# Performance work log

Measured on AMD Instinct MI355X. Metric: run time of the kernel, lower is better.

## Reference

```python
import jax, jax.numpy as jnp
import numpy as np

NG, CPN, K = 16, 24, 5          # ngroups, channels-per-group, kernel size
C = NG * CPN                     # 384 total channels
PAD = K // 2                     # PseudoEntropyPad(2, ...)


def build_mask():
    """PixelCNN-style group-causal mask for MaskConv2 (hidden/type-B: center
    position allows input group <= output group)."""
    m = np.zeros((C, C, K, K), np.float32)
    m[:, :, :PAD, :] = 1.0                      # rows above center: all allowed
    m[:, :, PAD, :PAD] = 1.0                    # center row, left of center
    g = np.arange(C) // CPN
    m[:, :, PAD, PAD] = (g[None, :] <= g[:, None]).astype(np.float32)
    return jnp.asarray(m)


def masked_conv(x, w, b, mask):
    # zero pad by 2 (PseudoEntropyPad) + VALID 5x5 conv == SAME conv
    y = jax.lax.conv_general_dilated(
        x, w * mask, window_strides=(1, 1), padding=[(PAD, PAD), (PAD, PAD)],
        dimension_numbers=("NCHW", "OIHW", "NCHW"))
    return y + b[None, :, None, None]


def prelu(x, a):
    return jnp.where(x >= 0, x, a[None, :, None, None] * x)


def setup_inputs() -> dict:
    key = jax.random.key(0)
    ks = jax.random.split(key, 5)
    x = jax.random.normal(ks[0], (2, C, 256, 512), dtype=jnp.float32)
    w1 = jax.random.normal(ks[1], (C, C, K, K), dtype=jnp.float32) * 0.02
    w2 = jax.random.normal(ks[2], (C, C, K, K), dtype=jnp.float32) * 0.02
    b1 = jnp.zeros((C,), jnp.float32)
    b2 = jnp.zeros((C,), jnp.float32)
    a1 = jnp.full((C,), 0.25, jnp.float32)   # PReLU init
    a2 = jnp.full((C,), 0.25, jnp.float32)
    return {"x": x, "w1": w1, "b1": b1, "a1": a1, "w2": w2, "b2": b2, "a2": a2}


def reference(x, w1, b1, a1, w2, b2, a2):
    mask = build_mask()
    y = prelu(masked_conv(x, w1, b1, mask), a1)   # EntropyConv 1 (pad+conv+PReLU+trim)
    y = prelu(masked_conv(y, w2, b2, mask), a2)   # EntropyConv 2
    return y + x                                   # residual
```

## Files before the change

### kernel.cpp

```cpp
#include <hip/hip_runtime.h>
#include <hip/hip_bf16.h>


#define C_CH 384
#define HH   256
#define WWD  512
#define NN   2
#define NKC  24
#define PR   260
#define PC   516
#define ICS16 (PR * PC * 16)
#define TCOLS 144
#define PLANE_SH (4 * TCOLS * 16)
#define TSH (2 * PLANE_SH)
#define TSTRIDE (NKC * C_CH * 16)
#define ICSTRIDE (2 * C_CH * 16)

typedef __attribute__((ext_vector_type(8)))  short short8;
typedef __attribute__((ext_vector_type(16))) float f32x16;

typedef const __attribute__((address_space(1))) void* gas_t;
typedef __attribute__((address_space(3))) void* las_t;

__device__ inline unsigned short f2bf(float f) {
    union { float f; unsigned int u; } v; v.f = f;
    unsigned int r = v.u + 0x7FFFu + ((v.u >> 16) & 1u);
    return (unsigned short)(r >> 16);
}

__global__ __launch_bounds__(256) void k_prepack(const float* __restrict__ w1, const float* __restrict__ w2,
                                                 unsigned short* __restrict__ wp1, unsigned short* __restrict__ wp2) {
    int idx = blockIdx.x * 256 + threadIdx.x;
    const int TOT = 13 * NKC * C_CH * 16;
    if (idx >= TOT) return;
    int iq = idx & 15;
    int o  = (idx >> 4) % C_CH;
    int kc = (idx / (16 * C_CH)) % NKC;
    int t  = idx / (16 * C_CH * NKC);
    int i  = kc * 16 + iq;
    int kh = t < 5 ? 0 : (t < 10 ? 1 : 2);
    int kw = t < 5 ? t : (t < 10 ? t - 5 : t - 10);
    bool keep = (t != 12) || ((i / 24) <= (o / 24));
    int src = ((o * C_CH + i) * 5 + kh) * 5 + kw;
    wp1[idx] = keep ? f2bf(w1[src]) : (unsigned short)0;
    wp2[idx] = keep ? f2bf(w2[src]) : (unsigned short)0;
}

__global__ __launch_bounds__(256) void k_zero_halo(unsigned short* __restrict__ a, unsigned short* __restrict__ b) {
    int plane = blockIdx.x;
    const short8 z = (short8){0,0,0,0,0,0,0,0};
    for (int bi = 0; bi < 2; ++bi) {
        unsigned short* p = (bi ? b : a) + (size_t)plane * ICS16;
        for (int i = threadIdx.x; i < 4128; i += 256) {
            int r4 = i / 1032;
            int rem = i - r4 * 1032;
            int row = r4 < 2 ? r4 : 254 + r4;
            *(short8*)&p[row * (PC * 16) + rem * 8] = z;
        }
        for (int i = threadIdx.x; i < 2048; i += 256) {
            int row = 2 + (i >> 3);
            int j = i & 7;
            int col = (j < 4) ? (j >> 1) : (512 + (j >> 1));
            int q = j & 1;
            *(short8*)&p[(row * PC + col) * 16 + q * 8] = z;
        }
    }
}

__global__ __launch_bounds__(256) void k_repack_x(const float* __restrict__ x, unsigned short* __restrict__ xc) {
    int bid = blockIdx.x;
    int w0 = (bid & 7) << 6;
    int h  = (bid >> 3) & 255;
    int n  = bid >> 11;
    int wi = threadIdx.x & 63;
    int cq = threadIdx.x >> 6;
    int w  = w0 + wi;
    int inb = n * C_CH * HH * WWD + h * WWD + w;
    for (int cc = 0; cc < 12; ++cc) {
        int c0 = cc * 32 + cq * 8;
        short8 outv;
        #pragma unroll
        for (int k = 0; k < 8; ++k) {
            float f = x[inb + (c0 + k) * (HH * WWD)];
            outv[k] = (short)f2bf(f);
        }
        int kc = cc * 2 + (cq >> 1);
        int oidx = (n * NKC + kc) * ICS16 + ((h + 2) * PC + (w + 2)) * 16 + (cq & 1) * 8;
        *(short8*)&xc[oidx] = outv;
    }
}

template<int SECOND>
__global__ __launch_bounds__(256, 2) void k_conv(const unsigned short* __restrict__ in,
                                                 const unsigned short* __restrict__ wp,
                                                 const float* __restrict__ bias,
                                                 const float* __restrict__ alpha,
                                                 const float* __restrict__ xres,
                                                 void* __restrict__ outp) {
    __shared__ __align__(16) unsigned short Xs[2][TSH];

    int bid0 = blockIdx.x;
    int xcd = bid0 & 7;
    int j0  = bid0 >> 3;
    int tile = xcd * 128 + j0 / 3;
    int ob   = j0 % 3;
    int n    = tile >> 9;
    int hp   = (tile >> 2) & 127;
    int wseg = tile & 3;
    int w0 = wseg << 7, o0 = ob << 7, h0 = hp << 1;

    int tid = threadIdx.x;
    int lane = tid & 63;
    int wv = tid >> 6;
    int wr = wv >> 1, wc = wv & 1;
    int lo5 = lane & 31, hi = lane >> 5;

    int goff[9];
    #pragma unroll
    for (int it = 0; it < 9; ++it) {
        int k = wv * 9 + it;
        int plane = k / 18;
        int s = (k % 18) * 64 + lane;
        int r = s / 288;
        int rem = s - r * 288;
        int col = rem >> 1, h16 = rem & 1;
        goff[it] = plane * ICS16 + ((h0 + r) * PC + (w0 + col)) * 16 + h16 * 8;
    }

    f32x16 acc[4][2];
    #pragma unroll
    for (int pt = 0; pt < 4; ++pt)
        #pragma unroll
        for (int ot = 0; ot < 2; ++ot)
            #pragma unroll
            for (int r = 0; r < 16; ++r) acc[pt][ot][r] = 0.f;

    const unsigned short* gbase_n = in + (size_t)n * NKC * ICS16;

    const int xlane = wr * (TCOLS * 16) + lo5 * 16 + hi * 8;
    const unsigned short* wpb = wp + (size_t)(o0 + wc * 64) * 16;
    const int wlane = lo5 * 16 + hi * 8;
    int woff0 = 0;
    int woff1 = C_CH * 16;

    const int KH[13] = {0,0,0,0,0,1,1,1,1,1,2,2,2};
    const int KW[13] = {0,1,2,3,4,0,1,2,3,4,0,1,2};

#define LOAD_XA(dst, u) do {                                              \
        const int t_ = (u) >> 1, hf_ = (u) & 1;                           \
        const int c0_ = hf_ * PLANE_SH + KH[t_] * (TCOLS * 16)            \
                      + KW[t_] * 16;                                      \
        _Pragma("unroll")                                                 \
        for (int pt_ = 0; pt_ < 4; ++pt_)                                 \
            (dst)[pt_] = *(const short8*)&xsp[xlane + c0_ + pt_ * 512];   \
    } while (0)

#define LOAD_WB(dst, woff) do {                                           \
        (dst)[0] = *(const short8*)&wpb[(woff) + wlane];                  \
        (dst)[1] = *(const short8*)&wpb[(woff) + wlane + 512];            \
    } while (0)

#define OCTET(xv, wv_) do {                                               \
        _Pragma("unroll")                                                 \
        for (int pt = 0; pt < 4; ++pt)                                    \
            _Pragma("unroll")                                             \
            for (int ot = 0; ot < 2; ++ot) {                              \
                if (SECOND)                                               \
                    acc[pt][ot] = __builtin_amdgcn_mfma_f32_32x32x16_bf16( \
                        (wv_)[ot], (xv)[pt], acc[pt][ot], 0, 0, 0);        \
                else                                                      \
                    acc[pt][ot] = __builtin_amdgcn_mfma_f32_32x32x16_bf16( \
                        (xv)[pt], (wv_)[ot], acc[pt][ot], 0, 0, 0);        \
            }                                                             \
    } while (0)

    short8 wb[2][2];
    LOAD_WB(wb[0], woff0);
    LOAD_WB(wb[1], woff1);

    #pragma unroll
    for (int it = 0; it < 9; ++it)
        __builtin_amdgcn_global_load_lds((gas_t)(gbase_n + goff[it]),
                                         (las_t)&Xs[0][(wv * 9 + it) * 512], 16, 0, 0);
    __syncthreads();

    for (int ic = 0; ic < 12; ++ic) {
        const unsigned short* xsp = &Xs[ic & 1][0];
        if (ic < 11) {
            const unsigned short* gb = gbase_n + (size_t)(ic + 1) * 2 * ICS16;
            #pragma unroll
            for (int it = 0; it < 9; ++it)
                __builtin_amdgcn_global_load_lds((gas_t)(gb + goff[it]),
                                                 (las_t)&Xs[(ic & 1) ^ 1][(wv * 9 + it) * 512], 16, 0, 0);
        }

        short8 xa[2][4];
        LOAD_XA(xa[0], 0);

        #pragma unroll
        for (int s2 = 0; s2 < 26; ++s2) {
            if (s2 + 1 < 26) LOAD_XA(xa[(s2 + 1) & 1], s2 + 1);
            __builtin_amdgcn_s_barrier();
            __builtin_amdgcn_s_setprio(1);
            OCTET(xa[s2 & 1], wb[s2 & 1]);
            __builtin_amdgcn_s_setprio(0);
            if (s2 + 2 < 26) {
                if ((s2 & 1) == 0) { woff0 += TSTRIDE; LOAD_WB(wb[0], woff0); }
                else               { woff1 += TSTRIDE; LOAD_WB(wb[1], woff1); }
            } else {
                if ((s2 & 1) == 0) { woff0 += ICSTRIDE - 12 * TSTRIDE; LOAD_WB(wb[0], woff0); }
                else               { woff1 += ICSTRIDE - 12 * TSTRIDE; LOAD_WB(wb[1], woff1); }
            }
        }
        __syncthreads();
    }
#undef LOAD_XA
#undef LOAD_WB
#undef OCTET

    int h = h0 + wr;
    if (!SECOND) {
        unsigned short* y = (unsigned short*)outp;
        #pragma unroll
        for (int ot = 0; ot < 2; ++ot) {
            int o = o0 + wc * 64 + ot * 32 + lo5;
            float bo = bias[o], ao = alpha[o];
            int kc = o >> 4;
            int o15 = o & 15;
            size_t base = (size_t)(n * NKC + kc) * ICS16 + ((h + 2) * PC + (w0 + 2)) * 16 + o15;
            #pragma unroll
            for (int pt = 0; pt < 4; ++pt) {
                #pragma unroll
                for (int reg = 0; reg < 16; ++reg) {
                    int p = pt * 32 + (reg & 3) + 8 * (reg >> 2) + 4 * hi;
                    float v = acc[pt][ot][reg] + bo;
                    v = v >= 0.f ? v : ao * v;
                    y[base + (size_t)p * 16] = f2bf(v);
                }
            }
        }
    } else {
        float* outf = (float*)outp;
        #pragma unroll
        for (int ot = 0; ot < 2; ++ot) {
            #pragma unroll
            for (int reg = 0; reg < 16; ++reg) {
                int o = o0 + wc * 64 + ot * 32 + (reg & 3) + 8 * (reg >> 2) + 4 * hi;
                float bo = bias[o], ao = alpha[o];
                #pragma unroll
                for (int pt = 0; pt < 4; ++pt) {
                    int w = w0 + pt * 32 + lo5;
                    float v = acc[pt][ot][reg] + bo;
                    v = v >= 0.f ? v : ao * v;
                    size_t idx = (size_t)((n * C_CH + o) * HH + h) * WWD + w;
                    outf[idx] = v + xres[idx];
                }
            }
        }
    }
}

extern "C" void kernel_launch(void* const* d_in, const int* in_sizes, int n_in,
                              void* d_out, int out_size, void* d_ws, size_t ws_size,
                              hipStream_t stream) {
    const float* x  = (const float*)d_in[0];
    const float* w1 = (const float*)d_in[1];
    const float* b1 = (const float*)d_in[2];
    const float* a1 = (const float*)d_in[3];
    const float* w2 = (const float*)d_in[4];
    const float* b2 = (const float*)d_in[5];
    const float* a2 = (const float*)d_in[6];

    const size_t PLANE_SHORTS = (size_t)NN * NKC * ICS16;
    unsigned short* xc  = (unsigned short*)d_out;
    unsigned short* yb  = (unsigned short*)d_ws;
    unsigned short* wp1 = yb + PLANE_SHORTS;
    unsigned short* wp2 = wp1 + 13 * NKC * C_CH * 16;

    k_prepack<<<(13 * NKC * C_CH * 16 + 255) / 256, 256, 0, stream>>>(w1, w2, wp1, wp2);
    k_zero_halo<<<NN * NKC, 256, 0, stream>>>(xc, yb);
    k_repack_x<<<NN * HH * (WWD / 64), 256, 0, stream>>>(x, xc);
    k_conv<0><<<3072, 256, 0, stream>>>(xc, wp1, b1, a1, nullptr, (void*)yb);
    k_conv<1><<<3072, 256, 0, stream>>>(yb, wp2, b2, a2, x, (void*)d_out);
}
```

Measured before the change: 1.801 ms.

## Shrink conv tile to one output row and stage per 16-channel chunk

The conv tile drops from two output rows by 128 columns to one row by 128 columns, and the grid doubles. Each wave now covers a 64-pixel by 64-channel quadrant, with half the accumulators. Input staging goes from two 16-channel planes per step to one plane over three rows, which shrinks LDS use and lets launch bounds target 4 blocks per SM. The aim is higher occupancy and better latency hiding, paid for with less reuse: each input row is now staged for only one output row, and weights are re-read twice as often per pixel.

```diff
diff --git a/kernel.cpp b/kernel.cpp
--- a/kernel.cpp
+++ b/kernel.cpp
@@ -10,11 +10,10 @@
 #define PR   260
 #define PC   516
 #define ICS16 (PR * PC * 16)
-#define TCOLS 144
-#define PLANE_SH (4 * TCOLS * 16)
-#define TSH (2 * PLANE_SH)
+#define TC3  160
+#define BUFSH (3 * TC3 * 16)
 #define TSTRIDE (NKC * C_CH * 16)
-#define ICSTRIDE (2 * C_CH * 16)
+#define CSTRIDE (C_CH * 16)
 
 typedef __attribute__((ext_vector_type(8)))  short short8;
 typedef __attribute__((ext_vector_type(16))) float f32x16;
@@ -91,45 +90,44 @@
 }
 
 template<int SECOND>
-__global__ __launch_bounds__(256, 2) void k_conv(const unsigned short* __restrict__ in,
+__global__ __launch_bounds__(256, 4) void k_conv(const unsigned short* __restrict__ in,
                                                  const unsigned short* __restrict__ wp,
                                                  const float* __restrict__ bias,
                                                  const float* __restrict__ alpha,
                                                  const float* __restrict__ xres,
                                                  void* __restrict__ outp) {
-    __shared__ __align__(16) unsigned short Xs[2][TSH];
+    __shared__ __align__(16) unsigned short Xs[2][BUFSH];
 
     int bid0 = blockIdx.x;
     int xcd = bid0 & 7;
     int j0  = bid0 >> 3;
-    int tile = xcd * 128 + j0 / 3;
+    int tile = xcd * 256 + j0 / 3;
     int ob   = j0 % 3;
-    int n    = tile >> 9;
-    int hp   = (tile >> 2) & 127;
     int wseg = tile & 3;
-    int w0 = wseg << 7, o0 = ob << 7, h0 = hp << 1;
+    int h0   = (tile >> 2) & 255;
+    int n    = tile >> 10;
+    int w0 = wseg << 7, o0 = ob << 7;
 
     int tid = threadIdx.x;
     int lane = tid & 63;
     int wv = tid >> 6;
-    int wr = wv >> 1, wc = wv & 1;
+    int pc = wv >> 1, oc = wv & 1;
     int lo5 = lane & 31, hi = lane >> 5;
 
-    int goff[9];
+    int goff[4];
     #pragma unroll
-    for (int it = 0; it < 9; ++it) {
-        int k = wv * 9 + it;
-        int plane = k / 18;
-        int s = (k % 18) * 64 + lane;
-        int r = s / 288;
-        int rem = s - r * 288;
-        int col = rem >> 1, h16 = rem & 1;
-        goff[it] = plane * ICS16 + ((h0 + r) * PC + (w0 + col)) * 16 + h16 * 8;
-    }
-
-    f32x16 acc[4][2];
+    for (int k = 0; k < 4; ++k) {
+        int i = wv + 4 * k;
+        int row = i / 5, cb = i % 5;
+        goff[k] = ((h0 + row) * PC + (w0 + cb * 32 + (lane >> 1))) * 16 + (lane & 1) * 8;
+    }
+
+    const int KH[13] = {0,0,0,0,0,1,1,1,1,1,2,2,2};
+    const int KW[13] = {0,1,2,3,4,0,1,2,3,4,0,1,2};
+
+    f32x16 acc[2][2];
     #pragma unroll
-    for (int pt = 0; pt < 4; ++pt)
+    for (int pt = 0; pt < 2; ++pt)
         #pragma unroll
         for (int ot = 0; ot < 2; ++ot)
             #pragma unroll
@@ -137,22 +135,27 @@
 
     const unsigned short* gbase_n = in + (size_t)n * NKC * ICS16;
 
-    const int xlane = wr * (TCOLS * 16) + lo5 * 16 + hi * 8;
-    const unsigned short* wpb = wp + (size_t)(o0 + wc * 64) * 16;
+    const int xlane = (pc * 64 + lo5) * 16 + hi * 8;
+    const unsigned short* wpb = wp + (size_t)(o0 + oc * 64) * 16;
     const int wlane = lo5 * 16 + hi * 8;
     int woff0 = 0;
-    int woff1 = C_CH * 16;
-
-    const int KH[13] = {0,0,0,0,0,1,1,1,1,1,2,2,2};
-    const int KW[13] = {0,1,2,3,4,0,1,2,3,4,0,1,2};
-
-#define LOAD_XA(dst, u) do {                                              \
-        const int t_ = (u) >> 1, hf_ = (u) & 1;                           \
-        const int c0_ = hf_ * PLANE_SH + KH[t_] * (TCOLS * 16)            \
-                      + KW[t_] * 16;                                      \
+    int woff1 = TSTRIDE;
+
+#define STAGE(kcn, b) do {                                                \
+        const unsigned short* gb_ = gbase_n + (size_t)(kcn) * ICS16;      \
         _Pragma("unroll")                                                 \
-        for (int pt_ = 0; pt_ < 4; ++pt_)                                 \
-            (dst)[pt_] = *(const short8*)&xsp[xlane + c0_ + pt_ * 512];   \
+        for (int k_ = 0; k_ < 4; ++k_) {                                  \
+            int i_ = wv + 4 * k_;                                         \
+            if (i_ < 15)                                                  \
+                __builtin_amdgcn_global_load_lds((gas_t)(gb_ + goff[k_]), \
+                    (las_t)&Xs[b][i_ * 512], 16, 0, 0);                   \
+        }                                                                 \
+    } while (0)
+
+#define LOAD_XA(dst, t_) do {                                             \
+        const int c0_ = (KH[t_] * TC3 + KW[t_]) * 16;                     \
+        (dst)[0] = *(const short8*)&xsp[xlane + c0_];                     \
+        (dst)[1] = *(const short8*)&xsp[xlane + c0_ + 512];               \
     } while (0)
 
 #define LOAD_WB(dst, woff) do {                                           \
@@ -160,79 +163,76 @@
         (dst)[1] = *(const short8*)&wpb[(woff) + wlane + 512];            \
     } while (0)
 
-#define OCTET(xv, wv_) do {                                               \
+#define QUAD(xv, wq) do {                                                 \
         _Pragma("unroll")                                                 \
-        for (int pt = 0; pt < 4; ++pt)                                    \
+        for (int pt = 0; pt < 2; ++pt)                                    \
             _Pragma("unroll")                                             \
             for (int ot = 0; ot < 2; ++ot) {                              \
                 if (SECOND)                                               \
                     acc[pt][ot] = __builtin_amdgcn_mfma_f32_32x32x16_bf16( \
-                        (wv_)[ot], (xv)[pt], acc[pt][ot], 0, 0, 0);        \
+                        (wq)[ot], (xv)[pt], acc[pt][ot], 0, 0, 0);         \
                 else                                                      \
                     acc[pt][ot] = __builtin_amdgcn_mfma_f32_32x32x16_bf16( \
-                        (xv)[pt], (wv_)[ot], acc[pt][ot], 0, 0, 0);        \
+                        (xv)[pt], (wq)[ot], acc[pt][ot], 0, 0, 0);         \
             }                                                             \
+    } while (0)
+
+#define HALF(bufi, wxor) do {                                             \
+        const unsigned short* xsp = &Xs[bufi][0];                         \
+        short8 xa[2][2];                                                  \
+        LOAD_XA(xa[0], 0);                                                \
+        _Pragma("unroll")                                                 \
+        for (int s2 = 0; s2 < 13; ++s2) {                                 \
+            if (s2 < 12) LOAD_XA(xa[(s2 + 1) & 1], s2 + 1);               \
+            __builtin_amdgcn_s_barrier();                                 \
+            __builtin_amdgcn_s_setprio(1);                                \
+            QUAD(xa[s2 & 1], wb[(s2 & 1) ^ (wxor)]);                      \
+            __builtin_amdgcn_s_setprio(0);                                \
+            if (((s2 & 1) ^ (wxor)) == 0) {                               \
+                woff0 += (s2 < 11) ? 2 * TSTRIDE : (CSTRIDE - 11 * TSTRIDE); \
+                LOAD_WB(wb[0], woff0);                                    \
+            } else {                                                      \
+                woff1 += (s2 < 11) ? 2 * TSTRIDE : (CSTRIDE - 11 * TSTRIDE); \
+                LOAD_WB(wb[1], woff1);                                    \
+            }                                                             \
+        }                                                                 \
     } while (0)
 
     short8 wb[2][2];
     LOAD_WB(wb[0], woff0);
     LOAD_WB(wb[1], woff1);
 
-    #pragma unroll
-    for (int it = 0; it < 9; ++it)
-        __builtin_amdgcn_global_load_lds((gas_t)(gbase_n + goff[it]),
-                                         (las_t)&Xs[0][(wv * 9 + it) * 512], 16, 0, 0);
+    STAGE(0, 0);
     __syncthreads();
 
-    for (int ic = 0; ic < 12; ++ic) {
-        const unsigned short* xsp = &Xs[ic & 1][0];
-        if (ic < 11) {
-            const unsigned short* gb = gbase_n + (size_t)(ic + 1) * 2 * ICS16;
-            #pragma unroll
-            for (int it = 0; it < 9; ++it)
-                __builtin_amdgcn_global_load_lds((gas_t)(gb + goff[it]),
-                                                 (las_t)&Xs[(ic & 1) ^ 1][(wv * 9 + it) * 512], 16, 0, 0);
-        }
-
-        short8 xa[2][4];
-        LOAD_XA(xa[0], 0);
-
-        #pragma unroll
-        for (int s2 = 0; s2 < 26; ++s2) {
-            if (s2 + 1 < 26) LOAD_XA(xa[(s2 + 1) & 1], s2 + 1);
-            __builtin_amdgcn_s_barrier();
-            __builtin_amdgcn_s_setprio(1);
-            OCTET(xa[s2 & 1], wb[s2 & 1]);
-            __builtin_amdgcn_s_setprio(0);
-            if (s2 + 2 < 26) {
-                if ((s2 & 1) == 0) { woff0 += TSTRIDE; LOAD_WB(wb[0], woff0); }
-                else               { woff1 += TSTRIDE; LOAD_WB(wb[1], woff1); }
-            } else {
-                if ((s2 & 1) == 0) { woff0 += ICSTRIDE - 12 * TSTRIDE; LOAD_WB(wb[0], woff0); }
-                else               { woff1 += ICSTRIDE - 12 * TSTRIDE; LOAD_WB(wb[1], woff1); }
-            }
-        }
+    for (int j = 0; j < 12; ++j) {
+        STAGE(2 * j + 1, 1);
+        HALF(0, 0);
         __syncthreads();
-    }
+        if (j < 11) STAGE(2 * j + 2, 0);
+        HALF(1, 1);
+        __syncthreads();
+    }
+#undef STAGE
 #undef LOAD_XA
 #undef LOAD_WB
-#undef OCTET
-
-    int h = h0 + wr;
+#undef QUAD
+#undef HALF
+
     if (!SECOND) {
         unsigned short* y = (unsigned short*)outp;
         #pragma unroll
         for (int ot = 0; ot < 2; ++ot) {
-            int o = o0 + wc * 64 + ot * 32 + lo5;
+            int o = o0 + oc * 64 + ot * 32 + lo5;
             float bo = bias[o], ao = alpha[o];
             int kc = o >> 4;
             int o15 = o & 15;
-            size_t base = (size_t)(n * NKC + kc) * ICS16 + ((h + 2) * PC + (w0 + 2)) * 16 + o15;
+            size_t base = (size_t)(n * NKC + kc) * ICS16 + ((h0 + 2) * PC + (w0 + 2)) * 16 + o15;
             #pragma unroll
-            for (int pt = 0; pt < 4; ++pt) {
+            for (int pt = 0; pt < 2; ++pt) {
                 #pragma unroll
                 for (int reg = 0; reg < 16; ++reg) {
-                    int p = pt * 32 + (reg & 3) + 8 * (reg >> 2) + 4 * hi;
+                    int p = pc * 64 + pt * 32 + (reg & 3) + 8 * (reg >> 2) + 4 * hi;
                     float v = acc[pt][ot][reg] + bo;
                     v = v >= 0.f ? v : ao * v;
                     y[base + (size_t)p * 16] = f2bf(v);
@@ -245,14 +245,14 @@
         for (int ot = 0; ot < 2; ++ot) {
             #pragma unroll
             for (int reg = 0; reg < 16; ++reg) {
-                int o = o0 + wc * 64 + ot * 32 + (reg & 3) + 8 * (reg >> 2) + 4 * hi;
+                int o = o0 + oc * 64 + ot * 32 + (reg & 3) + 8 * (reg >> 2) + 4 * hi;
                 float bo = bias[o], ao = alpha[o];
                 #pragma unroll
-                for (int pt = 0; pt < 4; ++pt) {
-                    int w = w0 + pt * 32 + lo5;
+                for (int pt = 0; pt < 2; ++pt) {
+                    int w = w0 + pc * 64 + pt * 32 + lo5;
                     float v = acc[pt][ot][reg] + bo;
                     v = v >= 0.f ? v : ao * v;
-                    size_t idx = (size_t)((n * C_CH + o) * HH + h) * WWD + w;
+                    size_t idx = (size_t)((n * C_CH + o) * HH + h0) * WWD + w;
                     outf[idx] = v + xres[idx];
                 }
             }
@@ -280,6 +280,6 @@
     k_prepack<<<(13 * NKC * C_CH * 16 + 255) / 256, 256, 0, stream>>>(w1, w2, wp1, wp2);
     k_zero_halo<<<NN * NKC, 256, 0, stream>>>(xc, yb);
     k_repack_x<<<NN * HH * (WWD / 64), 256, 0, stream>>>(x, xc);
-    k_conv<0><<<3072, 256, 0, stream>>>(xc, wp1, b1, a1, nullptr, (void*)yb);
-    k_conv<1><<<3072, 256, 0, stream>>>(yb, wp2, b2, a2, x, (void*)d_out);
-}
+    k_conv<0><<<6144, 256, 0, stream>>>(xc, wp1, b1, a1, nullptr, (void*)yb);
+    k_conv<1><<<6144, 256, 0, stream>>>(yb, wp2, b2, a2, x, (void*)d_out);
+}
```

After: 2.680 ms. +48.8%, slower.
